# Kernel tuning notes

Measured on AMD Instinct MI355X. Metric: run time of the kernel, lower is better.

Reference implementation:

```python
import jax, jax.numpy as jnp
import numpy as np

N, DIM, H, HD = 2048, 1280, 16, 80

def _rotate_half(x):
    x1, x2 = x[..., :x.shape[-1] // 2], x[..., x.shape[-1] // 2:]
    return jnp.concatenate((-x2, x1), axis=-1)

def setup_inputs() -> dict:
    key = jax.random.key(0)
    ks = jax.random.split(key, 6)
    hidden_states = jax.random.normal(ks[0], (N, DIM), dtype=jnp.float32)
    cu_seqlens = jnp.array([0, N // 2, N], dtype=jnp.int32)  # 2 packed segments
    # rotary embeddings: half-dim inverse frequencies, duplicated to head_dim
    inv_freq = 1.0 / (10000.0 ** (np.arange(0, HD // 2, dtype=np.float32) * 2.0 / HD))
    pos = np.arange(N, dtype=np.float32) % (N // 2)  # positions restart per segment
    freqs = pos[:, None] * inv_freq[None, :]           # [N, HD/2]
    emb = jnp.asarray(np.concatenate([freqs, freqs], axis=-1))  # [N, HD]
    cos, sin = jnp.cos(emb), jnp.sin(emb)
    Wqkv = jax.random.normal(ks[1], (DIM, 3 * DIM), dtype=jnp.float32) * (DIM ** -0.5)
    bqkv = jax.random.normal(ks[2], (3 * DIM,), dtype=jnp.float32) * 0.02
    Wproj = jax.random.normal(ks[3], (DIM, DIM), dtype=jnp.float32) * (DIM ** -0.5)
    bproj = jax.random.normal(ks[4], (DIM,), dtype=jnp.float32) * 0.02
    return {"hidden_states": hidden_states, "cu_seqlens": cu_seqlens,
            "cos": cos, "sin": sin, "Wqkv": Wqkv, "bqkv": bqkv,
            "Wproj": Wproj, "bproj": bproj}

def reference(hidden_states, cu_seqlens, cos, sin, Wqkv, bqkv, Wproj, bproj):
    n = hidden_states.shape[0]
    scale = HD ** -0.5
    qkv = (hidden_states @ Wqkv + bqkv).reshape(n, 3, H, HD)
    q, k, v = qkv[:, 0], qkv[:, 1], qkv[:, 2]           # each [N, H, HD]
    # RoPE (fp32), cos/sin broadcast over heads: [N, 1, HD]
    c, s = cos[:, None, :], sin[:, None, :]
    q = q * c + _rotate_half(q) * s
    k = k * c + _rotate_half(k) * s
    # block-diagonal varlen mask from cu_seqlens (per-segment full attention)
    seg_id = jnp.searchsorted(cu_seqlens, jnp.arange(n), side='right')  # [N]
    mask = seg_id[:, None] == seg_id[None, :]                           # [N, N]
    scores = jnp.einsum('qhd,khd->hqk', q, k) * scale                   # [H, N, N]
    scores = jnp.where(mask[None], scores, -jnp.inf)
    attn = jax.nn.softmax(scores.astype(jnp.float32), axis=-1).astype(q.dtype)
    out = jnp.einsum('hqk,khd->qhd', attn, v).reshape(n, H * HD)        # [N, DIM]
    return out @ Wproj + bproj
```

## Files before the change

### kernel.cpp

```cpp
#include <hip/hip_runtime.h>
#include <hip/hip_bf16.h>

constexpr int N_TOK  = 2048;
constexpr int DIM    = 1280;
constexpr int NHEAD  = 16;
constexpr int HD     = 80;
constexpr int QKV_N  = 3 * DIM;

using bf16 = __hip_bfloat16;
typedef __attribute__((ext_vector_type(4)))  float f32x4;
typedef __attribute__((ext_vector_type(16))) float f32x16;
typedef __attribute__((ext_vector_type(8)))  short short8;
typedef unsigned int uint;

__device__ __forceinline__ float b2f(bf16 x) { return __bfloat162float(x); }
__device__ __forceinline__ bf16  f2b(float x) { return __float2bfloat16(x); }

__device__ __forceinline__ uint pk2(float a, float b) {
  __align__(4) bf16 t[2] = {f2b(a), f2b(b)};
  return *reinterpret_cast<uint*>(t);
}

typedef const __attribute__((address_space(1))) unsigned int* gas_u32;
typedef __attribute__((address_space(3))) unsigned int* las_u32;
__device__ __forceinline__ void gload_lds16(const void* g, void* l) {
  __builtin_amdgcn_global_load_lds((gas_u32)g, (las_u32)l, 16, 0, 0);
}

__device__ __forceinline__ void transpose_body(const float* __restrict__ W,
                                               bf16* __restrict__ WT, int K, int N) {
  __shared__ float tile[32][33];
  const int n0 = blockIdx.x * 32, k0 = blockIdx.y * 32;
  const int tc = threadIdx.x & 31, tr = threadIdx.x >> 5;
#pragma unroll
  for (int r = tr; r < 32; r += 8)
    tile[r][tc] = W[(size_t)(k0 + r) * N + n0 + tc];
  __syncthreads();
#pragma unroll
  for (int r = tr; r < 32; r += 8)
    WT[(size_t)(n0 + r) * K + k0 + tc] = f2b(tile[tc][r]);
}

__global__ __launch_bounds__(256)
void prep_kernel(const float* __restrict__ hs, bf16* __restrict__ hsb,
                 const float* __restrict__ Wqkv, bf16* __restrict__ WqkvT,
                 const float* __restrict__ Wproj, bf16* __restrict__ WprojT) {
  if (blockIdx.z == 0) {
    const int bid = blockIdx.y * gridDim.x + blockIdx.x;
    if (bid >= (N_TOK * DIM) / 2048) return;
    const int i = bid * 2048 + threadIdx.x * 8;
    const float4 a = *reinterpret_cast<const float4*>(hs + i);
    const float4 b = *reinterpret_cast<const float4*>(hs + i + 4);
    __align__(16) bf16 w[8] = {f2b(a.x), f2b(a.y), f2b(a.z), f2b(a.w),
                               f2b(b.x), f2b(b.y), f2b(b.z), f2b(b.w)};
    *reinterpret_cast<short8*>(hsb + i) = *reinterpret_cast<const short8*>(w);
  } else if (blockIdx.z == 1) {
    transpose_body(Wqkv, WqkvT, DIM, QKV_N);
  } else {
    if (blockIdx.x >= DIM / 32) return;
    transpose_body(Wproj, WprojT, DIM, DIM);
  }
}

template <int OBF>
__global__ __launch_bounds__(256)
void mfma_gemm(const bf16* __restrict__ A, const bf16* __restrict__ BT,
               const float* __restrict__ bias, void* __restrict__ C,
               int M, int N, int K) {
  __shared__ bf16 As[128 * 64];
  __shared__ bf16 Bs[128 * 64];
  const int tid = threadIdx.x;
  const int wid = tid >> 6, lane = tid & 63;
  const int lm = lane & 15, kg = lane >> 4;
  const int wm = (wid >> 1) * 64, wn = (wid & 1) * 64;

  const int nblk = gridDim.x * gridDim.y;
  const int bid  = blockIdx.y * gridDim.x + blockIdx.x;
  const int lbid = (bid & 7) * (nblk >> 3) + (bid >> 3);
  const int m0 = (lbid / gridDim.x) * 128, n0 = (lbid % gridDim.x) * 128;

  const int srow = lane >> 3;
  const int sblk = (lane & 7) ^ srow;

  f32x4 acc[4][4];
#pragma unroll
  for (int i = 0; i < 4; ++i)
#pragma unroll
    for (int j = 0; j < 4; ++j) acc[i][j] = (f32x4){0.f, 0.f, 0.f, 0.f};

  for (int k0 = 0; k0 < K; k0 += 64) {
#pragma unroll
    for (int i = 0; i < 4; ++i) {
      const int slot = i * 4 + wid;
      const int row = slot * 8 + srow;
      gload_lds16(A + (size_t)(m0 + row) * K + k0 + sblk * 8, &As[slot * 512]);
      gload_lds16(BT + (size_t)(n0 + row) * K + k0 + sblk * 8, &Bs[slot * 512]);
    }
    __syncthreads();

#pragma unroll
    for (int kh = 0; kh < 2; ++kh) {
      short8 af[4], bfr[4];
#pragma unroll
      for (int t = 0; t < 4; ++t) {
        const int ar = wm + t * 16 + lm;
        af[t] = *reinterpret_cast<const short8*>(
            &As[ar * 64 + ((kh * 4 + kg) ^ (ar & 7)) * 8]);
        const int br = wn + t * 16 + lm;
        bfr[t] = *reinterpret_cast<const short8*>(
            &Bs[br * 64 + ((kh * 4 + kg) ^ (br & 7)) * 8]);
      }
#pragma unroll
      for (int mi = 0; mi < 4; ++mi)
#pragma unroll
        for (int ni = 0; ni < 4; ++ni)
          acc[mi][ni] = __builtin_amdgcn_mfma_f32_16x16x32_bf16(
              af[mi], bfr[ni], acc[mi][ni], 0, 0, 0);
    }
    __syncthreads();
  }

#pragma unroll
  for (int mi = 0; mi < 4; ++mi) {
#pragma unroll
    for (int ni = 0; ni < 4; ++ni) {
      const int col = n0 + wn + ni * 16 + lm;
      const float bv = bias[col];
#pragma unroll
      for (int r = 0; r < 4; ++r) {
        const int row = m0 + wm + mi * 16 + kg * 4 + r;
        const float v = acc[mi][ni][r] + bv;
        if constexpr (OBF)
          ((bf16*)C)[(size_t)row * N + col] = f2b(v);
        else
          ((float*)C)[(size_t)row * N + col] = v;
      }
    }
  }
}

__global__ __launch_bounds__(256)
void rope_k_kernel(bf16* __restrict__ qkv, const float* __restrict__ cosb,
                   const float* __restrict__ sinb) {
  const int idx = blockIdx.x * 256 + threadIdx.x;
  const int d0  = (idx % 5) * 8;
  const int h   = (idx / 5) % NHEAD;
  const int n   = idx / (5 * NHEAD);
  const size_t base = (size_t)n * QKV_N + DIM + h * HD;

  short8 a = *reinterpret_cast<const short8*>(qkv + base + d0);
  short8 b = *reinterpret_cast<const short8*>(qkv + base + 40 + d0);
  float cc1[8], cc2[8], ss1[8], ss2[8];
  *reinterpret_cast<float4*>(&cc1[0]) = *reinterpret_cast<const float4*>(cosb + n * HD + d0);
  *reinterpret_cast<float4*>(&cc1[4]) = *reinterpret_cast<const float4*>(cosb + n * HD + d0 + 4);
  *reinterpret_cast<float4*>(&cc2[0]) = *reinterpret_cast<const float4*>(cosb + n * HD + 40 + d0);
  *reinterpret_cast<float4*>(&cc2[4]) = *reinterpret_cast<const float4*>(cosb + n * HD + 44 + d0);
  *reinterpret_cast<float4*>(&ss1[0]) = *reinterpret_cast<const float4*>(sinb + n * HD + d0);
  *reinterpret_cast<float4*>(&ss1[4]) = *reinterpret_cast<const float4*>(sinb + n * HD + d0 + 4);
  *reinterpret_cast<float4*>(&ss2[0]) = *reinterpret_cast<const float4*>(sinb + n * HD + 40 + d0);
  *reinterpret_cast<float4*>(&ss2[4]) = *reinterpret_cast<const float4*>(sinb + n * HD + 44 + d0);

  __align__(16) bf16 o1[8], o2[8];
#pragma unroll
  for (int e = 0; e < 8; ++e) {
    const float x1 = b2f(reinterpret_cast<const bf16*>(&a)[e]);
    const float x2 = b2f(reinterpret_cast<const bf16*>(&b)[e]);
    o1[e] = f2b(x1 * cc1[e] - x2 * ss1[e]);
    o2[e] = f2b(x2 * cc2[e] + x1 * ss2[e]);
  }
  *reinterpret_cast<short8*>(qkv + base + d0)      = *reinterpret_cast<const short8*>(o1);
  *reinterpret_cast<short8*>(qkv + base + 40 + d0) = *reinterpret_cast<const short8*>(o2);
}

constexpr int KC   = 64;
constexpr int KSTR = 104;
constexpr int VSTR = 88;
constexpr int VROWS = 96;

__global__ __launch_bounds__(256)
void attn_mfma_kernel(const bf16* __restrict__ qkv, const int* __restrict__ cu,
                      const float* __restrict__ cosb, const float* __restrict__ sinb,
                      bf16* __restrict__ out, int nseg) {
  __shared__ bf16 Ks[2][KC * KSTR];
  __shared__ bf16 Vt[2][VROWS * VSTR];

  const int p = blockIdx.x;
  const int lidx = (p & 7) * (gridDim.x >> 3) + (p >> 3);
  const int xt  = lidx & 15;
  const int seg = (lidx >> 4) % nseg;
  const int h   = (lidx >> 4) / nseg;

  const int s0 = cu[seg], s1 = cu[seg + 1];
  if (s0 + xt * 128 >= s1) return;

  const int tid  = threadIdx.x;
  const int wid  = tid >> 6, lane = tid & 63;
  const int l31  = lane & 31;
  const int half = lane >> 5;
  const float scale = 0.11180339887498949f;

  const int qrow = s0 + xt * 128 + wid * 32 + l31;

#pragma unroll
  for (int t = 0; t < 2; ++t) {
    const int s = tid + t * 256;
    if (s < 352) {
      const int b = s / 176, rem = s % 176;
      const int r = 80 + rem / 11, sl = rem % 11;
      *reinterpret_cast<short8*>(&Vt[b][r * VSTR + sl * 8]) =
          (short8){0, 0, 0, 0, 0, 0, 0, 0};
    }
  }

  short8 qraw[5];
  const int nclamp = min(qrow, s1 - 1);
#pragma unroll
  for (int j = 0; j < 5; ++j) {
    const int dbase = j * 16 + half * 8;
    qraw[j] = (qrow < s1)
        ? *reinterpret_cast<const short8*>(qkv + (size_t)qrow * QKV_N + h * HD + dbase)
        : (short8){0, 0, 0, 0, 0, 0, 0, 0};
  }
  short8 part[5];
#pragma unroll
  for (int w = 0; w < 4; ++w) {
    const uint d0 = reinterpret_cast<const uint*>(&qraw[0])[w];
    const uint d1 = reinterpret_cast<const uint*>(&qraw[1])[w];
    const uint d2 = reinterpret_cast<const uint*>(&qraw[2])[w];
    const uint d3 = reinterpret_cast<const uint*>(&qraw[3])[w];
    const uint d4 = reinterpret_cast<const uint*>(&qraw[4])[w];
    auto s1p = __builtin_amdgcn_permlane32_swap(d2, d0, false, false);
    auto s2p = __builtin_amdgcn_permlane32_swap(d4, d2, false, false);
    auto s3p = __builtin_amdgcn_permlane32_swap(d0, d3, false, false);
    auto s4p = __builtin_amdgcn_permlane32_swap(d3, d1, false, false);
    auto s5p = __builtin_amdgcn_permlane32_swap(d1, d4, false, false);
    reinterpret_cast<uint*>(&part[0])[w] = half ? s3p[0] : s1p[1];
    reinterpret_cast<uint*>(&part[1])[w] = half ? s5p[0] : s4p[1];
    reinterpret_cast<uint*>(&part[2])[w] = half ? s1p[0] : s2p[1];
    reinterpret_cast<uint*>(&part[3])[w] = half ? s4p[0] : s3p[1];
    reinterpret_cast<uint*>(&part[4])[w] = half ? s2p[0] : s5p[1];
  }
  short8 qa[5];
  {
    const float* cq = cosb + nclamp * HD;
    const float* sq = sinb + nclamp * HD;
#pragma unroll
    for (int j = 0; j < 5; ++j) {
      const int dbase = j * 16 + half * 8;
      float cv[8], sv[8];
      *reinterpret_cast<float4*>(&cv[0]) = *reinterpret_cast<const float4*>(cq + dbase);
      *reinterpret_cast<float4*>(&cv[4]) = *reinterpret_cast<const float4*>(cq + dbase + 4);
      *reinterpret_cast<float4*>(&sv[0]) = *reinterpret_cast<const float4*>(sq + dbase);
      *reinterpret_cast<float4*>(&sv[4]) = *reinterpret_cast<const float4*>(sq + dbase + 4);
      const float sgn = (dbase < 40) ? -1.f : 1.f;
      __align__(16) bf16 o[8];
#pragma unroll
      for (int e = 0; e < 8; ++e) {
        const float x  = b2f(reinterpret_cast<const bf16*>(&qraw[j])[e]);
        const float xp = b2f(reinterpret_cast<const bf16*>(&part[j])[e]);
        o[e] = f2b(x * cv[e] + sgn * xp * sv[e]);
      }
      qa[j] = *reinterpret_cast<const short8*>(o);
    }
  }

  short8 kreg[3], vreg[4];
  const int vgrp = tid / 10, vsl = tid % 10;
  auto issueK = [&](int c) {
    const int k0 = s0 + c * KC;
#pragma unroll
    for (int t = 0; t < 3; ++t) {
      const int s = tid + t * 256;
      if (s < 640) {
        const int r = min(k0 + s / 10, s1 - 1);
        kreg[t] = *reinterpret_cast<const short8*>(
            qkv + (size_t)r * QKV_N + DIM + h * HD + (s % 10) * 8);
      }
    }
  };
  auto commitK = [&](int buf) {
#pragma unroll
    for (int t = 0; t < 3; ++t) {
      const int s = tid + t * 256;
      if (s < 640)
        *reinterpret_cast<short8*>(&Ks[buf][(s / 10) * KSTR + (s % 10) * 8]) =
            kreg[t];
    }
  };
  auto issueV = [&](int c) {
    if (tid < 160) {
      const int k0 = s0 + c * KC;
#pragma unroll
      for (int e = 0; e < 4; ++e) {
        const int r = min(k0 + vgrp * 4 + e, s1 - 1);
        vreg[e] = *reinterpret_cast<const short8*>(
            qkv + (size_t)r * QKV_N + 2 * DIM + h * HD + vsl * 8);
      }
    }
  };
  auto commitV = [&](int buf) {
    if (tid < 160) {
      const int r0 = vgrp * 4;
      const int swz = (vsl & 7) << 3;
#pragma unroll
      for (int de = 0; de < 8; ++de) {
        __align__(8) bf16 w[4] = {reinterpret_cast<const bf16*>(&vreg[0])[de],
                                  reinterpret_cast<const bf16*>(&vreg[1])[de],
                                  reinterpret_cast<const bf16*>(&vreg[2])[de],
                                  reinterpret_cast<const bf16*>(&vreg[3])[de]};
        *reinterpret_cast<uint2*>(&Vt[buf][(vsl * 8 + de) * VSTR + (r0 ^ swz)]) =
            *reinterpret_cast<const uint2*>(w);
      }
    }
  };

  f32x16 oacc[3];
#pragma unroll
  for (int dt = 0; dt < 3; ++dt)
#pragma unroll
    for (int r = 0; r < 16; ++r) oacc[dt][r] = 0.f;
  float m = -1e30f, l = 0.f;
  const int nch = (s1 - s0 + KC - 1) / KC;

  issueK(0);
  issueV(0);
  commitK(0);
  commitV(0);
  if (nch > 1) {
    issueK(1);
    issueV(1);
  }
  __syncthreads();

  for (int c = 0; c < nch; ++c) {
    const int cur = c & 1;
    const int nk = min(KC, s1 - (s0 + c * KC));

    f32x16 sc[2];
    __builtin_amdgcn_s_setprio(1);
#pragma unroll
    for (int kt = 0; kt < 2; ++kt) {
#pragma unroll
      for (int r = 0; r < 16; ++r) sc[kt][r] = 0.f;
#pragma unroll
      for (int ck = 0; ck < 5; ++ck) {
        short8 ka = *reinterpret_cast<const short8*>(
            &Ks[cur][(kt * 32 + l31) * KSTR + ck * 16 + half * 8]);
        sc[kt] = __builtin_amdgcn_mfma_f32_32x32x16_bf16(ka, qa[ck], sc[kt], 0, 0, 0);
      }
    }
    __builtin_amdgcn_s_setprio(0);

    if (c + 1 < nch) {
      commitK(cur ^ 1);
      commitV(cur ^ 1);
    }
    if (c + 2 < nch) {
      issueK(c + 2);
      issueV(c + 2);
    }

#pragma unroll
    for (int kt = 0; kt < 2; ++kt)
#pragma unroll
      for (int r = 0; r < 16; ++r) sc[kt][r] *= scale;
    if (nk < KC) {
#pragma unroll
      for (int kt = 0; kt < 2; ++kt)
#pragma unroll
        for (int r = 0; r < 16; ++r) {
          const int key = kt * 32 + (r & 3) + 8 * (r >> 2) + 4 * half;
          if (key >= nk) sc[kt][r] = -1e30f;
        }
    }
    float rml = sc[0][0];
#pragma unroll
    for (int kt = 0; kt < 2; ++kt)
#pragma unroll
      for (int r = 0; r < 16; ++r)
        if (kt | r) rml = fmaxf(rml, sc[kt][r]);
    if (!__all(rml - m <= 8.0f)) {
      float rm = fmaxf(rml, __shfl_xor(rml, 32));
      const float mnew = fmaxf(m, rm);
      const float fs = __expf(m - mnew);
      m = mnew;
      l *= fs;
#pragma unroll
      for (int dt = 0; dt < 3; ++dt)
#pragma unroll
        for (int r = 0; r < 16; ++r) oacc[dt][r] *= fs;
    }
#pragma unroll
    for (int kt = 0; kt < 2; ++kt)
#pragma unroll
      for (int r = 0; r < 16; ++r) {
        sc[kt][r] = __expf(sc[kt][r] - m);
        l += sc[kt][r];
      }

    uint pbw[4][4];
#pragma unroll
    for (int kt = 0; kt < 2; ++kt) {
      uint w[8];
#pragma unroll
      for (int i = 0; i < 8; ++i) w[i] = pk2(sc[kt][2 * i], sc[kt][2 * i + 1]);
#pragma unroll
      for (int kc2 = 0; kc2 < 2; ++kc2) {
        auto r02 = __builtin_amdgcn_permlane32_swap(w[4 * kc2 + 0],
                                                    w[4 * kc2 + 2], false, false);
        auto r13 = __builtin_amdgcn_permlane32_swap(w[4 * kc2 + 1],
                                                    w[4 * kc2 + 3], false, false);
        pbw[kt * 2 + kc2][0] = r02[0];
        pbw[kt * 2 + kc2][1] = r13[0];
        pbw[kt * 2 + kc2][2] = r02[1];
        pbw[kt * 2 + kc2][3] = r13[1];
      }
    }

    __builtin_amdgcn_s_setprio(1);
#pragma unroll
    for (int kc = 0; kc < 4; ++kc) {
      short8 pb = *reinterpret_cast<const short8*>(&pbw[kc][0]);
#pragma unroll
      for (int dt = 0; dt < 3; ++dt) {
        const int d = dt * 32 + l31;
        short8 va = *reinterpret_cast<const short8*>(
            &Vt[cur][d * VSTR + ((kc * 16 + half * 8) ^ (((d >> 3) & 7) << 3))]);
        oacc[dt] = __builtin_amdgcn_mfma_f32_32x32x16_bf16(va, pb, oacc[dt], 0, 0, 0);
      }
    }
    __builtin_amdgcn_s_setprio(0);

    __syncthreads();
  }

  l += __shfl_xor(l, 32);
  if (qrow < s1) {
    const float inv = 1.f / l;
    bf16* op = out + (size_t)qrow * DIM + h * HD;
#pragma unroll
    for (int dt = 0; dt < 3; ++dt) {
#pragma unroll
      for (int g = 0; g < 4; ++g) {
        const int d = dt * 32 + g * 8 + half * 4;
        if (d < HD) {
          __align__(8) bf16 w[4] = {f2b(oacc[dt][g * 4 + 0] * inv),
                                    f2b(oacc[dt][g * 4 + 1] * inv),
                                    f2b(oacc[dt][g * 4 + 2] * inv),
                                    f2b(oacc[dt][g * 4 + 3] * inv)};
          *reinterpret_cast<uint2*>(op + d) = *reinterpret_cast<const uint2*>(w);
        }
      }
    }
  }
}

extern "C" void kernel_launch(void* const* d_in, const int* in_sizes, int n_in,
                              void* d_out, int out_size, void* d_ws, size_t ws_size,
                              hipStream_t stream) {
  const float* hs    = (const float*)d_in[0];
  const int*   cu    = (const int*)d_in[1];
  const float* cosb  = (const float*)d_in[2];
  const float* sinb  = (const float*)d_in[3];
  const float* Wqkv  = (const float*)d_in[4];
  const float* bqkv  = (const float*)d_in[5];
  const float* Wproj = (const float*)d_in[6];
  const float* bproj = (const float*)d_in[7];

  bf16* qkv      = (bf16*)d_ws;
  bf16* attn_out = qkv + (size_t)N_TOK * QKV_N;
  bf16* WqkvT    = attn_out + (size_t)N_TOK * DIM;
  bf16* WprojT   = WqkvT + (size_t)QKV_N * DIM;
  bf16* hsb      = WprojT + (size_t)DIM * DIM;

  prep_kernel<<<dim3(QKV_N / 32, DIM / 32, 3), 256, 0, stream>>>(
      hs, hsb, Wqkv, WqkvT, Wproj, WprojT);

  mfma_gemm<1><<<dim3(QKV_N / 128, N_TOK / 128), 256, 0, stream>>>(
      hsb, WqkvT, bqkv, qkv, N_TOK, QKV_N, DIM);

  rope_k_kernel<<<(N_TOK * NHEAD * 5) / 256, 256, 0, stream>>>(qkv, cosb, sinb);

  int nseg = in_sizes[1] - 1;
  int nblk = (N_TOK / 128) * nseg * NHEAD;
  attn_mfma_kernel<<<nblk, 256, 0, stream>>>(qkv, cu, cosb, sinb, attn_out, nseg);

  mfma_gemm<0><<<dim3(DIM / 128, N_TOK / 128), 256, 0, stream>>>(
      attn_out, WprojT, bproj, d_out, N_TOK, DIM, DIM);
}
```

Baseline: 112.3 us.

## Software-pipeline QK^T of next chunk with softmax/PV of current chunk

Restructures the attention loop so the QK^T MFMAs for chunk c+1 are issued before the softmax and PV step of chunk c, using two ping-ponged score register sets. V shared memory becomes triple-buffered with a tighter stride and no padding rows; out-of-range head-dim rows are clamped and zeroed in registers instead of being zeroed in LDS. The goal is to overlap matrix work with the exp/softmax ALU work and to cut LDS padding. In exchange it holds more live accumulator registers, which may lower occupancy or cause spills.

Result: slower. 116.0 us (+3.3%).

```diff
diff --git a/kernel.cpp b/kernel.cpp
--- a/kernel.cpp
+++ b/kernel.cpp
@@ -174,15 +174,14 @@
 
 constexpr int KC   = 64;
 constexpr int KSTR = 104;
-constexpr int VSTR = 88;
-constexpr int VROWS = 96;
+constexpr int VSTR = 72;
 
 __global__ __launch_bounds__(256)
 void attn_mfma_kernel(const bf16* __restrict__ qkv, const int* __restrict__ cu,
                       const float* __restrict__ cosb, const float* __restrict__ sinb,
                       bf16* __restrict__ out, int nseg) {
   __shared__ bf16 Ks[2][KC * KSTR];
-  __shared__ bf16 Vt[2][VROWS * VSTR];
+  __shared__ bf16 Vt[3][HD * VSTR];
 
   const int p = blockIdx.x;
   const int lidx = (p & 7) * (gridDim.x >> 3) + (p >> 3);
@@ -200,17 +199,6 @@
   const float scale = 0.11180339887498949f;
 
   const int qrow = s0 + xt * 128 + wid * 32 + l31;
-
-#pragma unroll
-  for (int t = 0; t < 2; ++t) {
-    const int s = tid + t * 256;
-    if (s < 352) {
-      const int b = s / 176, rem = s % 176;
-      const int r = 80 + rem / 11, sl = rem % 11;
-      *reinterpret_cast<short8*>(&Vt[b][r * VSTR + sl * 8]) =
-          (short8){0, 0, 0, 0, 0, 0, 0, 0};
-    }
-  }
 
   short8 qraw[5];
   const int nclamp = min(qrow, s1 - 1);
@@ -322,21 +310,8 @@
   float m = -1e30f, l = 0.f;
   const int nch = (s1 - s0 + KC - 1) / KC;
 
-  issueK(0);
-  issueV(0);
-  commitK(0);
-  commitV(0);
-  if (nch > 1) {
-    issueK(1);
-    issueV(1);
-  }
-  __syncthreads();
-
-  for (int c = 0; c < nch; ++c) {
-    const int cur = c & 1;
-    const int nk = min(KC, s1 - (s0 + c * KC));
-
-    f32x16 sc[2];
+  auto qk_step = [&](int c, f32x16 (&sc)[2]) {
+    const int kb = c & 1;
     __builtin_amdgcn_s_setprio(1);
 #pragma unroll
     for (int kt = 0; kt < 2; ++kt) {
@@ -345,21 +320,15 @@
 #pragma unroll
       for (int ck = 0; ck < 5; ++ck) {
         short8 ka = *reinterpret_cast<const short8*>(
-            &Ks[cur][(kt * 32 + l31) * KSTR + ck * 16 + half * 8]);
+            &Ks[kb][(kt * 32 + l31) * KSTR + ck * 16 + half * 8]);
         sc[kt] = __builtin_amdgcn_mfma_f32_32x32x16_bf16(ka, qa[ck], sc[kt], 0, 0, 0);
       }
     }
     __builtin_amdgcn_s_setprio(0);
-
-    if (c + 1 < nch) {
-      commitK(cur ^ 1);
-      commitV(cur ^ 1);
-    }
-    if (c + 2 < nch) {
-      issueK(c + 2);
-      issueV(c + 2);
-    }
-
+  };
+
+  auto sm_pv_step = [&](int c, f32x16 (&sc)[2]) {
+    const int nk = min(KC, s1 - (s0 + c * KC));
 #pragma unroll
     for (int kt = 0; kt < 2; ++kt)
 #pragma unroll
@@ -397,7 +366,6 @@
         sc[kt][r] = __expf(sc[kt][r] - m);
         l += sc[kt][r];
       }
-
     uint pbw[4][4];
 #pragma unroll
     for (int kt = 0; kt < 2; ++kt) {
@@ -416,7 +384,7 @@
         pbw[kt * 2 + kc2][3] = r13[1];
       }
     }
-
+    const int vb = c % 3;
     __builtin_amdgcn_s_setprio(1);
 #pragma unroll
     for (int kc = 0; kc < 4; ++kc) {
@@ -424,14 +392,54 @@
 #pragma unroll
       for (int dt = 0; dt < 3; ++dt) {
         const int d = dt * 32 + l31;
+        const int dc = min(d, HD - 1);
         short8 va = *reinterpret_cast<const short8*>(
-            &Vt[cur][d * VSTR + ((kc * 16 + half * 8) ^ (((d >> 3) & 7) << 3))]);
+            &Vt[vb][dc * VSTR + ((kc * 16 + half * 8) ^ (((dc >> 3) & 7) << 3))]);
+        if (d >= HD) va = (short8){0, 0, 0, 0, 0, 0, 0, 0};
         oacc[dt] = __builtin_amdgcn_mfma_f32_32x32x16_bf16(va, pb, oacc[dt], 0, 0, 0);
       }
     }
     __builtin_amdgcn_s_setprio(0);
-
+  };
+
+  f32x16 scA[2], scB[2];
+
+  issueK(0);
+  issueV(0);
+  commitK(0);
+  commitV(0);
+  if (nch > 1) {
+    issueK(1);
+    issueV(1);
+  }
+  __syncthreads();
+  qk_step(0, scA);
+  if (nch > 1) {
+    commitK(1);
+    commitV(1);
+  }
+  if (nch > 2) {
+    issueK(2);
+    issueV(2);
+  }
+  __syncthreads();
+
+  auto iter = [&](int c, f32x16 (&cur)[2], f32x16 (&nxt)[2]) {
+    if (c + 1 < nch) qk_step(c + 1, nxt);
+    sm_pv_step(c, cur);
+    if (c + 2 < nch) {
+      commitK((c + 2) & 1);
+      commitV((c + 2) % 3);
+    }
+    if (c + 3 < nch) {
+      issueK(c + 3);
+      issueV(c + 3);
+    }
     __syncthreads();
+  };
+  for (int c = 0; c < nch; c += 2) {
+    iter(c, scA, scB);
+    if (c + 1 < nch) iter(c + 1, scB, scA);
   }
 
   l += __shfl_xor(l, 32);
```
